# Kernel optimization log

Hardware: AMD Instinct MI355X
Metric: run time of the kernel (lower is better)

Reference implementation:

```python
import jax, jax.numpy as jnp
import numpy as np

INF = 1e38  # matches torch source constant


def setup_inputs() -> dict:
    key = jax.random.key(0)
    k1, k2, k3 = jax.random.split(key, 3)
    B, N, D = 16, 2048, 512
    query = jax.random.normal(k1, (B, N, D), dtype=jnp.float32)
    # nn.Linear(dims, dims, bias=False): weight [out, in] = [D, D]
    W_in = jax.random.normal(k2, (D, D), dtype=jnp.float32) * (1.0 / np.sqrt(D))
    # nn.Linear(2*dims, dims, bias=False): weight [D, 2D]
    W_out = jax.random.normal(k3, (D, 2 * D), dtype=jnp.float32) * (1.0 / np.sqrt(2 * D))
    return {"query": query, "W_in": W_in, "W_out": W_out}


def reference(query, W_in, W_out):
    B, N, D = query.shape
    # linear_in: y = x @ W^T
    q = jnp.einsum("bnd,ed->bne", query, W_in)  # [B, N, D]
    # full QK^T scores
    scores = jnp.einsum("bnd,bmd->bnm", q, q)  # [B, N, N]
    # torch: scores[:, triu_mask] = -INF  -> mask upper triangle INCLUDING diagonal
    mask = jnp.triu(jnp.ones((N, N), dtype=bool))
    scores = jnp.where(mask, -INF, scores)
    weights = jax.nn.softmax(scores, axis=-1)
    # row 0 is all -INF -> softmax gives uniform; torch zeroes it explicitly
    weights = weights.at[:, 0, :].set(0.0)
    mix = jnp.einsum("bnm,bmd->bnd", weights, q)  # [B, N, D]
    combined = jnp.concatenate([mix, q], axis=-1)  # [B, N, 2D]
    # linear_out (no activation since activation=None)
    output = jnp.einsum("bnc,dc->bnd", combined, W_out)  # [B, N, D]
    return output
```

## Files before the change

kernel.cpp:

```cpp
#include <hip/hip_runtime.h>

typedef _Float16 f16;
typedef _Float16 half8 __attribute__((ext_vector_type(8)));
typedef _Float16 half4 __attribute__((ext_vector_type(4)));
typedef float floatx4 __attribute__((ext_vector_type(4)));

#define MFMA16(a, b, c) __builtin_amdgcn_mfma_f32_16x16x32_f16(a, b, c, 0, 0, 0)

#define PHASE_WAIT_8()  do { asm volatile("s_waitcnt vmcnt(8)" ::: "memory"); \
    __builtin_amdgcn_sched_barrier(0); __builtin_amdgcn_s_barrier(); } while (0)
#define PHASE_WAIT_0()  do { asm volatile("s_waitcnt vmcnt(0)" ::: "memory"); \
    __builtin_amdgcn_sched_barrier(0); __builtin_amdgcn_s_barrier(); } while (0)

__device__ __forceinline__ void gload16(const void* g, void* l) {
    __builtin_amdgcn_global_load_lds((const __attribute__((address_space(1))) void*)g,
                                     (__attribute__((address_space(3))) void*)l, 16, 0, 0);
}

__global__ __launch_bounds__(256) void k_cvt(const float* __restrict__ query,
                                             const float* __restrict__ Wi,
                                             const float* __restrict__ Wo,
                                             f16* __restrict__ q16,
                                             f16* __restrict__ W16)
{
    int i = blockIdx.x * 256 + threadIdx.x;
    const float4* src;
    f16* dst;
    if (i < 4194304) { src = (const float4*)query + i; dst = q16 + (size_t)i * 4; }
    else if (i < 4259840) { int j = i - 4194304; src = (const float4*)Wi + j; dst = W16 + (size_t)j * 4; }
    else { int j = i - 4259840; src = (const float4*)Wo + j; dst = W16 + 262144 + (size_t)j * 4; }
    float4 v = *src;
    half4 h = {(f16)v.x, (f16)v.y, (f16)v.z, (f16)v.w};
    *reinterpret_cast<half4*>(dst) = h;
}

__global__ __launch_bounds__(256) void k_qin(const f16* __restrict__ q16,
                                             const f16* __restrict__ W16,
                                             f16* __restrict__ comb,
                                             f16* __restrict__ qT)
{
    __shared__ char sm[65536];
    const int tid = threadIdx.x, lane = tid & 63, w = tid >> 6;
    const int l15 = lane & 15, quad = lane >> 4;
    const int id = blockIdx.x, xcd = id & 7, u = id >> 3;
    const int mbase = (xcd * 32 + (u >> 2)) * 128;
    const int nbase = (u & 3) * 128;
    const int wm = (w & 1) * 64, wn = (w >> 1) * 64;
    const int ia = wm >> 4, jb = wn >> 4;

    floatx4 acc[4][4];
#pragma unroll
    for (int i = 0; i < 4; ++i)
#pragma unroll
        for (int j = 0; j < 4; ++j) acc[i][j] = (floatx4)0.f;

    auto STAGE = [&](int k0, int bsel) {
        f16* At = (f16*)(sm + bsel * 32768);
        f16* Bt = At + 8192;
#pragma unroll
        for (int jr = 0; jr < 4; ++jr) {
            int bi = jr * 4 + w, i2 = bi >> 1, s = bi & 1;
            gload16(q16 + (size_t)(mbase + i2 * 16 + l15) * 512 + k0 + s * 32 + quad * 8, At + bi * 512);
            gload16(W16 + (size_t)(nbase + i2 * 16 + l15) * 512 + k0 + s * 32 + quad * 8, Bt + bi * 512);
        }
    };

    STAGE(0, 0);
    STAGE(64, 1);
    for (int it = 0; it < 8; ++it) {
        const int cur = it & 1;
        if (it < 7) PHASE_WAIT_8(); else PHASE_WAIT_0();
        f16* At = (f16*)(sm + cur * 32768);
        f16* Bt = At + 8192;
#pragma unroll
        for (int s = 0; s < 2; ++s) {
            half8 a[4], bf[4];
#pragma unroll
            for (int i = 0; i < 4; ++i)
                a[i] = *reinterpret_cast<half8*>(At + ((ia + i) * 2 + s) * 512 + lane * 8);
#pragma unroll
            for (int j = 0; j < 4; ++j)
                bf[j] = *reinterpret_cast<half8*>(Bt + ((jb + j) * 2 + s) * 512 + lane * 8);
#pragma unroll
            for (int i = 0; i < 4; ++i)
#pragma unroll
                for (int j = 0; j < 4; ++j)
                    acc[i][j] = MFMA16(a[i], bf[j], acc[i][j]);
        }
        __builtin_amdgcn_s_barrier();
        if (it + 2 < 8) STAGE((it + 2) * 64, cur);
    }
    const int bb = mbase >> 11, tb = mbase & 2047;
    f16* ct = (f16*)sm;
#pragma unroll
    for (int i = 0; i < 4; ++i)
#pragma unroll
        for (int j = 0; j < 4; ++j)
#pragma unroll
            for (int r = 0; r < 4; ++r)
                ct[(wm + i * 16 + quad * 4 + r) * 136 + wn + j * 16 + l15] = (f16)acc[i][j][r];
    __syncthreads();
#pragma unroll
    for (int it = 0; it < 8; ++it) {
        int c = it * 256 + tid, r = c >> 4, c8 = (c & 15) << 3;
        *reinterpret_cast<half8*>(comb + (size_t)(mbase + r) * 1024 + 512 + nbase + c8) =
            *reinterpret_cast<half8*>(ct + r * 136 + c8);
    }
    __syncthreads();
#pragma unroll
    for (int i = 0; i < 4; ++i)
#pragma unroll
        for (int j = 0; j < 4; ++j) {
            half4 h = {(f16)acc[i][j][0], (f16)acc[i][j][1], (f16)acc[i][j][2], (f16)acc[i][j][3]};
            *reinterpret_cast<half4*>(ct + (wn + j * 16 + l15) * 136 + wm + i * 16 + quad * 4) = h;
        }
    __syncthreads();
#pragma unroll
    for (int it = 0; it < 8; ++it) {
        int c = it * 256 + tid, dd = c >> 4, tc = (c & 15) << 3;
        *reinterpret_cast<half8*>(qT + ((size_t)bb * 512 + nbase + dd) * 2048 + tb + tc) =
            *reinterpret_cast<half8*>(ct + dd * 136 + tc);
    }
}

__global__ __launch_bounds__(256) void k_sgemmsm(const f16* __restrict__ comb,
                                                 f16* __restrict__ Pd,
                                                 float* __restrict__ Mt,
                                                 float* __restrict__ Lt)
{
    __shared__ char sm[65536];
    const int tid = threadIdx.x, lane = tid & 63, w = tid >> 6;
    const int l15 = lane & 15, quad = lane >> 4;
    const int wm = (w & 1) * 64, wn = (w >> 1) * 64;
    const int ia = wm >> 4, jb = wn >> 4;

    int bx = blockIdx.y, mt = 0;
    while ((mt + 1) * (mt + 2) / 2 <= bx) ++mt;
    const int nt = bx - mt * (mt + 1) / 2;
    const int b = blockIdx.x;
    const f16* qa = comb + ((size_t)b * 2048 + mt * 128) * 1024 + 512;
    const f16* qb = comb + ((size_t)b * 2048 + nt * 128) * 1024 + 512;

    floatx4 acc[4][4];
#pragma unroll
    for (int i = 0; i < 4; ++i)
#pragma unroll
        for (int j = 0; j < 4; ++j) acc[i][j] = (floatx4)0.f;

    auto STAGE = [&](int k0, int bsel) {
        f16* At = (f16*)(sm + bsel * 32768);
        f16* Bt = At + 8192;
#pragma unroll
        for (int jr = 0; jr < 4; ++jr) {
            int bi = jr * 4 + w, i2 = bi >> 1, s = bi & 1;
            gload16(qa + (size_t)(i2 * 16 + l15) * 1024 + k0 + s * 32 + quad * 8, At + bi * 512);
            gload16(qb + (size_t)(i2 * 16 + l15) * 1024 + k0 + s * 32 + quad * 8, Bt + bi * 512);
        }
    };

    STAGE(0, 0);
    STAGE(64, 1);
    for (int it = 0; it < 8; ++it) {
        const int cur = it & 1;
        if (it < 7) PHASE_WAIT_8(); else PHASE_WAIT_0();
        f16* At = (f16*)(sm + cur * 32768);
        f16* Bt = At + 8192;
#pragma unroll
        for (int s = 0; s < 2; ++s) {
            half8 a[4], bf[4];
#pragma unroll
            for (int i = 0; i < 4; ++i)
                a[i] = *reinterpret_cast<half8*>(At + ((ia + i) * 2 + s) * 512 + lane * 8);
#pragma unroll
            for (int j = 0; j < 4; ++j)
                bf[j] = *reinterpret_cast<half8*>(Bt + ((jb + j) * 2 + s) * 512 + lane * 8);
#pragma unroll
            for (int i = 0; i < 4; ++i)
#pragma unroll
                for (int j = 0; j < 4; ++j)
                    acc[i][j] = MFMA16(a[i], bf[j], acc[i][j]);
        }
        __builtin_amdgcn_s_barrier();
        if (it + 2 < 8) STAGE((it + 2) * 64, cur);
    }

    const bool diag = (nt == mt);
    f16* ct = (f16*)sm;
    float* redm = (float*)(sm + 40960);
    float* reds = (float*)(sm + 43008);
    const int hb = w & 1;

    float wmax[4][4];
#pragma unroll
    for (int i = 0; i < 4; ++i)
#pragma unroll
        for (int r = 0; r < 4; ++r) {
            const int rowl = wm + i * 16 + quad * 4 + r;
            float mm = -1e38f;
#pragma unroll
            for (int j = 0; j < 4; ++j) {
                float v = acc[i][j][r];
                if (diag && (wn + j * 16 + l15) >= rowl) v = -1e38f;
                mm = fmaxf(mm, v);
            }
            mm = fmaxf(mm, __shfl_xor(mm, 1));
            mm = fmaxf(mm, __shfl_xor(mm, 2));
            mm = fmaxf(mm, __shfl_xor(mm, 4));
            mm = fmaxf(mm, __shfl_xor(mm, 8));
            wmax[i][r] = mm;
        }
    if (l15 == 0)
#pragma unroll
        for (int i = 0; i < 4; ++i)
#pragma unroll
            for (int r = 0; r < 4; ++r)
                redm[w * 64 + i * 16 + quad * 4 + r] = wmax[i][r];
    __syncthreads();

#pragma unroll
    for (int i = 0; i < 4; ++i)
#pragma unroll
        for (int r = 0; r < 4; ++r) {
            const int idx = i * 16 + quad * 4 + r;
            const int rowl = wm + idx;
            const float m = fmaxf(redm[hb * 64 + idx], redm[(hb + 2) * 64 + idx]);
            float ssum = 0.f;
#pragma unroll
            for (int j = 0; j < 4; ++j) {
                const int col = wn + j * 16 + l15;
                const bool valid = !diag || (col < rowl);
                float e = valid ? __expf(acc[i][j][r] - m) : 0.f;
                ssum += e;
                ct[rowl * 136 + col] = (f16)e;
            }
            ssum += __shfl_xor(ssum, 1);
            ssum += __shfl_xor(ssum, 2);
            ssum += __shfl_xor(ssum, 4);
            ssum += __shfl_xor(ssum, 8);
            wmax[i][r] = ssum;
        }
    if (l15 == 0)
#pragma unroll
        for (int i = 0; i < 4; ++i)
#pragma unroll
            for (int r = 0; r < 4; ++r)
                reds[w * 64 + i * 16 + quad * 4 + r] = wmax[i][r];
    __syncthreads();

    if (tid < 128) {
        const int h2 = tid >> 6, i2 = tid & 63;
        const float mm = fmaxf(redm[h2 * 64 + i2], redm[(h2 + 2) * 64 + i2]);
        const float ll = reds[h2 * 64 + i2] + reds[(h2 + 2) * 64 + i2];
        const size_t o = (((size_t)b * 16 + nt) << 11) + mt * 128 + tid;
        Mt[o] = mm;
        Lt[o] = ll;
    }
    f16* Pt = Pd + ((size_t)(b * 136 + bx) << 14);
#pragma unroll
    for (int itp = 0; itp < 8; ++itp) {
        int c = itp * 256 + tid, r_ = c >> 4, c8 = (c & 15) << 3;
        *reinterpret_cast<half8*>(Pt + r_ * 128 + c8) =
            *reinterpret_cast<half8*>(ct + r_ * 136 + c8);
    }
}

__global__ __launch_bounds__(256) void k_stats(float* Mt, const float* __restrict__ Lt)
{
    const int b = blockIdx.x, row = blockIdx.y * 256 + threadIdx.x;
    const int mtr = row >> 7;
    float mv[16], lv[16];
    for (int t = 0; t <= mtr; ++t) {
        const size_t o = (((size_t)b * 16 + t) << 11) + row;
        mv[t] = Mt[o];
        lv[t] = Lt[o];
    }
    float M = -1e38f;
    for (int t = 0; t <= mtr; ++t) M = fmaxf(M, mv[t]);
    float l = 0.f;
    for (int t = 0; t <= mtr; ++t) l += lv[t] * __expf(mv[t] - M);
    const float invl = (l > 0.f) ? 1.f / l : 0.f;
    for (int t = 0; t <= mtr; ++t)
        Mt[(((size_t)b * 16 + t) << 11) + row] = __expf(mv[t] - M) * invl;
}

__global__ __launch_bounds__(256) void k_pscale(f16* __restrict__ Pd,
                                               const float* __restrict__ Ft)
{
    int bx = blockIdx.y, mt = 0;
    while ((mt + 1) * (mt + 2) / 2 <= bx) ++mt;
    const int nt = bx - mt * (mt + 1) / 2;
    const int b = blockIdx.x;
    const int tid = threadIdx.x;
    const int row = tid >> 1, c0 = (tid & 1) * 64;
    const float Fv = Ft[(((size_t)b * 16 + nt) << 11) + mt * 128 + row];
    f16* Pt = Pd + ((size_t)(b * 136 + bx) << 14) + (size_t)row * 128 + c0;
#pragma unroll
    for (int c = 0; c < 8; ++c) {
        half8 h = *reinterpret_cast<half8*>(Pt + c * 8);
#pragma unroll
        for (int e = 0; e < 8; ++e) h[e] = (f16)((float)h[e] * Fv);
        *reinterpret_cast<half8*>(Pt + c * 8) = h;
    }
}

__global__ __launch_bounds__(256) void k_pv(const f16* __restrict__ Pd,
                                            const f16* __restrict__ qT,
                                            f16* __restrict__ comb)
{
    __shared__ char sm[65536];
    const int tid = threadIdx.x, lane = tid & 63, w = tid >> 6;
    const int l15 = lane & 15, quad = lane >> 4;
    const int wm = (w & 1) * 64, wn = (w >> 1) * 64;
    const int ia = wm >> 4, jb = wn >> 4;
    const int id = blockIdx.x;
    const int p = id & 7, nb = (id >> 3) & 3, b = id >> 5;
    const f16* Pdb = Pd + ((size_t)b * 136 << 14);
    const f16* qTb = qT + ((size_t)b * 512 + nb * 128) * 2048;

    for (int t = 0; t < 2; ++t) {
        const int mt = t ? (15 - p) : p;
        const int tb0 = mt * (mt + 1) / 2;
        const int kit = (mt + 1) * 2;

        floatx4 acc[4][4];
#pragma unroll
        for (int i = 0; i < 4; ++i)
#pragma unroll
            for (int j = 0; j < 4; ++j) acc[i][j] = (floatx4)0.f;

        auto STAGE = [&](int it, int bsel) {
            f16* At = (f16*)(sm + bsel * 32768);
            f16* Bt = At + 8192;
            const int k0 = it * 64;
#pragma unroll
            for (int jr = 0; jr < 4; ++jr) {
                int bi = jr * 4 + w, i2 = bi >> 1, s = bi & 1;
                gload16(Pdb + ((size_t)(tb0 + (k0 >> 7)) << 14) + (size_t)(i2 * 16 + l15) * 128
                            + (k0 & 64) + s * 32 + quad * 8,
                        At + bi * 512);
                gload16(qTb + (size_t)(i2 * 16 + l15) * 2048 + k0 + s * 32 + quad * 8, Bt + bi * 512);
            }
        };

        STAGE(0, 0);
        STAGE(1, 1);
        for (int it = 0; it < kit; ++it) {
            const int cur = it & 1;
            if (it < kit - 1) PHASE_WAIT_8(); else PHASE_WAIT_0();
            f16* At = (f16*)(sm + cur * 32768);
            f16* Bt = At + 8192;
#pragma unroll
            for (int s = 0; s < 2; ++s) {
                half8 a[4], bf[4];
#pragma unroll
                for (int i = 0; i < 4; ++i)
                    a[i] = *reinterpret_cast<half8*>(At + ((ia + i) * 2 + s) * 512 + lane * 8);
#pragma unroll
                for (int j = 0; j < 4; ++j)
                    bf[j] = *reinterpret_cast<half8*>(Bt + ((jb + j) * 2 + s) * 512 + lane * 8);
#pragma unroll
                for (int i = 0; i < 4; ++i)
#pragma unroll
                    for (int j = 0; j < 4; ++j)
                        acc[i][j] = MFMA16(a[i], bf[j], acc[i][j]);
            }
            __builtin_amdgcn_s_barrier();
            if (it + 2 < kit) STAGE(it + 2, cur);
        }

        f16* ct = (f16*)sm;
#pragma unroll
        for (int i = 0; i < 4; ++i)
#pragma unroll
            for (int j = 0; j < 4; ++j)
#pragma unroll
                for (int r = 0; r < 4; ++r)
                    ct[(wm + i * 16 + quad * 4 + r) * 136 + wn + j * 16 + l15] = (f16)acc[i][j][r];
        __syncthreads();
#pragma unroll
        for (int it = 0; it < 8; ++it) {
            int c = it * 256 + tid, r = c >> 4, c8 = (c & 15) << 3;
            *reinterpret_cast<half8*>(comb + ((size_t)b * 2048 + mt * 128 + r) * 1024 + nb * 128 + c8) =
                *reinterpret_cast<half8*>(ct + r * 136 + c8);
        }
        __syncthreads();
    }
}

__global__ __launch_bounds__(256) void k_out(const f16* __restrict__ comb,
                                             const f16* __restrict__ Wo16,
                                             float* __restrict__ out)
{
    __shared__ char sm[65536];
    const int tid = threadIdx.x, lane = tid & 63, w = tid >> 6;
    const int l15 = lane & 15, quad = lane >> 4;
    const int id = blockIdx.x, xcd = id & 7, u = id >> 3;
    const int mbase = (xcd * 32 + (u >> 2)) * 128;
    const int nbase = (u & 3) * 128;
    const int wm = (w & 1) * 64, wn = (w >> 1) * 64;
    const int ia = wm >> 4, jb = wn >> 4;

    floatx4 acc[4][4];
#pragma unroll
    for (int i = 0; i < 4; ++i)
#pragma unroll
        for (int j = 0; j < 4; ++j) acc[i][j] = (floatx4)0.f;

    auto STAGE = [&](int k0, int bsel) {
        f16* At = (f16*)(sm + bsel * 32768);
        f16* Bt = At + 8192;
#pragma unroll
        for (int jr = 0; jr < 4; ++jr) {
            int bi = jr * 4 + w, i2 = bi >> 1, s = bi & 1;
            gload16(comb + (size_t)(mbase + i2 * 16 + l15) * 1024 + k0 + s * 32 + quad * 8,
                    At + bi * 512);
            gload16(Wo16 + (size_t)(nbase + i2 * 16 + l15) * 1024 + k0 + s * 32 + quad * 8,
                    Bt + bi * 512);
        }
    };

    STAGE(0, 0);
    STAGE(64, 1);
    for (int it = 0; it < 16; ++it) {
        const int cur = it & 1;
        if (it < 15) PHASE_WAIT_8(); else PHASE_WAIT_0();
        f16* At = (f16*)(sm + cur * 32768);
        f16* Bt = At + 8192;
#pragma unroll
        for (int s = 0; s < 2; ++s) {
            half8 a[4], bf[4];
#pragma unroll
            for (int i = 0; i < 4; ++i)
                a[i] = *reinterpret_cast<half8*>(At + ((ia + i) * 2 + s) * 512 + lane * 8);
#pragma unroll
            for (int j = 0; j < 4; ++j)
                bf[j] = *reinterpret_cast<half8*>(Bt + ((jb + j) * 2 + s) * 512 + lane * 8);
#pragma unroll
            for (int i = 0; i < 4; ++i)
#pragma unroll
                for (int j = 0; j < 4; ++j)
                    acc[i][j] = MFMA16(a[i], bf[j], acc[i][j]);
        }
        __builtin_amdgcn_s_barrier();
        if (it + 2 < 16) STAGE((it + 2) * 64, cur);
    }
    float* cf = (float*)sm;
    for (int pass = 0; pass < 2; ++pass) {
        __syncthreads();
        if ((w & 1) == pass) {
#pragma unroll
            for (int i = 0; i < 4; ++i)
#pragma unroll
                for (int j = 0; j < 4; ++j)
#pragma unroll
                    for (int r = 0; r < 4; ++r)
                        cf[(i * 16 + quad * 4 + r) * 132 + wn + j * 16 + l15] = acc[i][j][r];
        }
        __syncthreads();
#pragma unroll
        for (int it = 0; it < 8; ++it) {
            int c = it * 256 + tid, row = c >> 5, c4 = (c & 31) << 2;
            __builtin_nontemporal_store(
                *reinterpret_cast<floatx4*>(cf + row * 132 + c4),
                reinterpret_cast<floatx4*>(out + (size_t)(mbase + pass * 64 + row) * 512 + nbase + c4));
        }
    }
}

extern "C" void kernel_launch(void* const* d_in, const int* in_sizes, int n_in,
                              void* d_out, int out_size, void* d_ws, size_t ws_size,
                              hipStream_t stream)
{
    const float* query = (const float*)d_in[0];
    const float* W_in  = (const float*)d_in[1];
    const float* W_out = (const float*)d_in[2];
    float* out = (float*)d_out;

    const size_t XOFF = 102236160ull;
    f16* comb = (f16*)d_ws;
    f16* qT   = comb + (size_t)32768 * 1024;
    f16* W16  = qT + (size_t)16 * 512 * 2048;
    f16* q16  = (f16*)((char*)d_ws + XOFF);
    f16* Pd   = (f16*)((char*)d_ws + XOFF);
    float* Mt = (float*)((char*)d_ws + XOFF + 71303168ull);
    float* Lt = (float*)((char*)d_ws + XOFF + 73400320ull);

    k_cvt<<<17152, 256, 0, stream>>>(query, W_in, W_out, q16, W16);
    k_qin<<<1024, 256, 0, stream>>>(q16, W16, comb, qT);
    k_sgemmsm<<<dim3(16, 136), 256, 0, stream>>>(comb, Pd, Mt, Lt);
    k_stats<<<dim3(16, 8), 256, 0, stream>>>(Mt, Lt);
    k_pscale<<<dim3(16, 136), 256, 0, stream>>>(Pd, Mt);
    k_pv<<<512, 256, 0, stream>>>(Pd, qT, comb);
    k_out<<<1024, 256, 0, stream>>>(comb, W16 + 262144, out);
}
```

Baseline: 404.5 us.

## Use 8 waves per block with 64x32 warp tiles in GEMM kernels

Switches the four MFMA GEMM kernels from 256 to 512 threads per block, halving each wave's output tile to 64x32 and its accumulator count, and splits staging loads across eight waves so the vmcnt wait drops to 4. The softmax row reductions in the score kernel now combine four column-wave partials instead of two. The aim is more waves in flight to hide LDS and global latency, in exchange for lower per-wave MFMA reuse (more LDS reads per FLOP) and more barrier participants.

```diff
diff --git a/kernel.cpp b/kernel.cpp
--- a/kernel.cpp
+++ b/kernel.cpp
@@ -7,7 +7,7 @@
 
 #define MFMA16(a, b, c) __builtin_amdgcn_mfma_f32_16x16x32_f16(a, b, c, 0, 0, 0)
 
-#define PHASE_WAIT_8()  do { asm volatile("s_waitcnt vmcnt(8)" ::: "memory"); \
+#define PHASE_WAIT_4()  do { asm volatile("s_waitcnt vmcnt(4)" ::: "memory"); \
     __builtin_amdgcn_sched_barrier(0); __builtin_amdgcn_s_barrier(); } while (0)
 #define PHASE_WAIT_0()  do { asm volatile("s_waitcnt vmcnt(0)" ::: "memory"); \
     __builtin_amdgcn_sched_barrier(0); __builtin_amdgcn_s_barrier(); } while (0)
@@ -16,6 +16,7 @@
     __builtin_amdgcn_global_load_lds((const __attribute__((address_space(1))) void*)g,
                                      (__attribute__((address_space(3))) void*)l, 16, 0, 0);
 }
+
 
 __global__ __launch_bounds__(256) void k_cvt(const float* __restrict__ query,
                                              const float* __restrict__ Wi,
@@ -34,10 +35,10 @@
     *reinterpret_cast<half4*>(dst) = h;
 }
 
-__global__ __launch_bounds__(256) void k_qin(const f16* __restrict__ q16,
-                                             const f16* __restrict__ W16,
-                                             f16* __restrict__ comb,
-                                             f16* __restrict__ qT)
+__global__ __launch_bounds__(512, 4) void k_qin(const f16* __restrict__ q16,
+                                                const f16* __restrict__ W16,
+                                                f16* __restrict__ comb,
+                                                f16* __restrict__ qT)
 {
     __shared__ char sm[65536];
     const int tid = threadIdx.x, lane = tid & 63, w = tid >> 6;
@@ -45,21 +46,21 @@
     const int id = blockIdx.x, xcd = id & 7, u = id >> 3;
     const int mbase = (xcd * 32 + (u >> 2)) * 128;
     const int nbase = (u & 3) * 128;
-    const int wm = (w & 1) * 64, wn = (w >> 1) * 64;
-    const int ia = wm >> 4, jb = wn >> 4;
-
-    floatx4 acc[4][4];
-#pragma unroll
-    for (int i = 0; i < 4; ++i)
-#pragma unroll
-        for (int j = 0; j < 4; ++j) acc[i][j] = (floatx4)0.f;
+    const int wm = (w & 1) * 64, wn = (w >> 1) * 32;
+    const int ia = (w & 1) * 4, jb = (w >> 1) * 2;
+
+    floatx4 acc[4][2];
+#pragma unroll
+    for (int i = 0; i < 4; ++i)
+#pragma unroll
+        for (int j = 0; j < 2; ++j) acc[i][j] = (floatx4)0.f;
 
     auto STAGE = [&](int k0, int bsel) {
         f16* At = (f16*)(sm + bsel * 32768);
         f16* Bt = At + 8192;
 #pragma unroll
-        for (int jr = 0; jr < 4; ++jr) {
-            int bi = jr * 4 + w, i2 = bi >> 1, s = bi & 1;
+        for (int jr = 0; jr < 2; ++jr) {
+            int bi = jr * 8 + w, i2 = bi >> 1, s = bi & 1;
             gload16(q16 + (size_t)(mbase + i2 * 16 + l15) * 512 + k0 + s * 32 + quad * 8, At + bi * 512);
             gload16(W16 + (size_t)(nbase + i2 * 16 + l15) * 512 + k0 + s * 32 + quad * 8, Bt + bi * 512);
         }
@@ -69,22 +70,22 @@
     STAGE(64, 1);
     for (int it = 0; it < 8; ++it) {
         const int cur = it & 1;
-        if (it < 7) PHASE_WAIT_8(); else PHASE_WAIT_0();
+        if (it < 7) PHASE_WAIT_4(); else PHASE_WAIT_0();
         f16* At = (f16*)(sm + cur * 32768);
         f16* Bt = At + 8192;
 #pragma unroll
         for (int s = 0; s < 2; ++s) {
-            half8 a[4], bf[4];
+            half8 a[4], bf[2];
 #pragma unroll
             for (int i = 0; i < 4; ++i)
                 a[i] = *reinterpret_cast<half8*>(At + ((ia + i) * 2 + s) * 512 + lane * 8);
 #pragma unroll
-            for (int j = 0; j < 4; ++j)
+            for (int j = 0; j < 2; ++j)
                 bf[j] = *reinterpret_cast<half8*>(Bt + ((jb + j) * 2 + s) * 512 + lane * 8);
 #pragma unroll
             for (int i = 0; i < 4; ++i)
 #pragma unroll
-                for (int j = 0; j < 4; ++j)
+                for (int j = 0; j < 2; ++j)
                     acc[i][j] = MFMA16(a[i], bf[j], acc[i][j]);
         }
         __builtin_amdgcn_s_barrier();
@@ -95,14 +96,14 @@
 #pragma unroll
     for (int i = 0; i < 4; ++i)
 #pragma unroll
-        for (int j = 0; j < 4; ++j)
+        for (int j = 0; j < 2; ++j)
 #pragma unroll
             for (int r = 0; r < 4; ++r)
                 ct[(wm + i * 16 + quad * 4 + r) * 136 + wn + j * 16 + l15] = (f16)acc[i][j][r];
     __syncthreads();
 #pragma unroll
-    for (int it = 0; it < 8; ++it) {
-        int c = it * 256 + tid, r = c >> 4, c8 = (c & 15) << 3;
+    for (int it = 0; it < 4; ++it) {
+        int c = it * 512 + tid, r = c >> 4, c8 = (c & 15) << 3;
         *reinterpret_cast<half8*>(comb + (size_t)(mbase + r) * 1024 + 512 + nbase + c8) =
             *reinterpret_cast<half8*>(ct + r * 136 + c8);
     }
@@ -110,29 +111,29 @@
 #pragma unroll
     for (int i = 0; i < 4; ++i)
 #pragma unroll
-        for (int j = 0; j < 4; ++j) {
+        for (int j = 0; j < 2; ++j) {
             half4 h = {(f16)acc[i][j][0], (f16)acc[i][j][1], (f16)acc[i][j][2], (f16)acc[i][j][3]};
             *reinterpret_cast<half4*>(ct + (wn + j * 16 + l15) * 136 + wm + i * 16 + quad * 4) = h;
         }
     __syncthreads();
 #pragma unroll
-    for (int it = 0; it < 8; ++it) {
-        int c = it * 256 + tid, dd = c >> 4, tc = (c & 15) << 3;
+    for (int it = 0; it < 4; ++it) {
+        int c = it * 512 + tid, dd = c >> 4, tc = (c & 15) << 3;
         *reinterpret_cast<half8*>(qT + ((size_t)bb * 512 + nbase + dd) * 2048 + tb + tc) =
             *reinterpret_cast<half8*>(ct + dd * 136 + tc);
     }
 }
 
-__global__ __launch_bounds__(256) void k_sgemmsm(const f16* __restrict__ comb,
-                                                 f16* __restrict__ Pd,
-                                                 float* __restrict__ Mt,
-                                                 float* __restrict__ Lt)
+__global__ __launch_bounds__(512, 4) void k_sgemmsm(const f16* __restrict__ comb,
+                                                    f16* __restrict__ Pd,
+                                                    float* __restrict__ Mt,
+                                                    float* __restrict__ Lt)
 {
     __shared__ char sm[65536];
     const int tid = threadIdx.x, lane = tid & 63, w = tid >> 6;
     const int l15 = lane & 15, quad = lane >> 4;
-    const int wm = (w & 1) * 64, wn = (w >> 1) * 64;
-    const int ia = wm >> 4, jb = wn >> 4;
+    const int wm = (w & 1) * 64, wn = (w >> 1) * 32;
+    const int ia = (w & 1) * 4, jb = (w >> 1) * 2;
 
     int bx = blockIdx.y, mt = 0;
     while ((mt + 1) * (mt + 2) / 2 <= bx) ++mt;
@@ -141,18 +142,18 @@
     const f16* qa = comb + ((size_t)b * 2048 + mt * 128) * 1024 + 512;
     const f16* qb = comb + ((size_t)b * 2048 + nt * 128) * 1024 + 512;
 
-    floatx4 acc[4][4];
-#pragma unroll
-    for (int i = 0; i < 4; ++i)
-#pragma unroll
-        for (int j = 0; j < 4; ++j) acc[i][j] = (floatx4)0.f;
+    floatx4 acc[4][2];
+#pragma unroll
+    for (int i = 0; i < 4; ++i)
+#pragma unroll
+        for (int j = 0; j < 2; ++j) acc[i][j] = (floatx4)0.f;
 
     auto STAGE = [&](int k0, int bsel) {
         f16* At = (f16*)(sm + bsel * 32768);
         f16* Bt = At + 8192;
 #pragma unroll
-        for (int jr = 0; jr < 4; ++jr) {
-            int bi = jr * 4 + w, i2 = bi >> 1, s = bi & 1;
+        for (int jr = 0; jr < 2; ++jr) {
+            int bi = jr * 8 + w, i2 = bi >> 1, s = bi & 1;
             gload16(qa + (size_t)(i2 * 16 + l15) * 1024 + k0 + s * 32 + quad * 8, At + bi * 512);
             gload16(qb + (size_t)(i2 * 16 + l15) * 1024 + k0 + s * 32 + quad * 8, Bt + bi * 512);
         }
@@ -162,22 +163,22 @@
     STAGE(64, 1);
     for (int it = 0; it < 8; ++it) {
         const int cur = it & 1;
-        if (it < 7) PHASE_WAIT_8(); else PHASE_WAIT_0();
+        if (it < 7) PHASE_WAIT_4(); else PHASE_WAIT_0();
         f16* At = (f16*)(sm + cur * 32768);
         f16* Bt = At + 8192;
 #pragma unroll
         for (int s = 0; s < 2; ++s) {
-            half8 a[4], bf[4];
+            half8 a[4], bf[2];
 #pragma unroll
             for (int i = 0; i < 4; ++i)
                 a[i] = *reinterpret_cast<half8*>(At + ((ia + i) * 2 + s) * 512 + lane * 8);
 #pragma unroll
-            for (int j = 0; j < 4; ++j)
+            for (int j = 0; j < 2; ++j)
                 bf[j] = *reinterpret_cast<half8*>(Bt + ((jb + j) * 2 + s) * 512 + lane * 8);
 #pragma unroll
             for (int i = 0; i < 4; ++i)
 #pragma unroll
-                for (int j = 0; j < 4; ++j)
+                for (int j = 0; j < 2; ++j)
                     acc[i][j] = MFMA16(a[i], bf[j], acc[i][j]);
         }
         __builtin_amdgcn_s_barrier();
@@ -186,8 +187,8 @@
 
     const bool diag = (nt == mt);
     f16* ct = (f16*)sm;
-    float* redm = (float*)(sm + 40960);
-    float* reds = (float*)(sm + 43008);
+    float* redm = (float*)(sm + 34816);
+    float* reds = (float*)(sm + 36864);
     const int hb = w & 1;
 
     float wmax[4][4];
@@ -198,7 +199,7 @@
             const int rowl = wm + i * 16 + quad * 4 + r;
             float mm = -1e38f;
 #pragma unroll
-            for (int j = 0; j < 4; ++j) {
+            for (int j = 0; j < 2; ++j) {
                 float v = acc[i][j][r];
                 if (diag && (wn + j * 16 + l15) >= rowl) v = -1e38f;
                 mm = fmaxf(mm, v);
@@ -223,10 +224,11 @@
         for (int r = 0; r < 4; ++r) {
             const int idx = i * 16 + quad * 4 + r;
             const int rowl = wm + idx;
-            const float m = fmaxf(redm[hb * 64 + idx], redm[(hb + 2) * 64 + idx]);
+            const float m = fmaxf(fmaxf(redm[hb * 64 + idx], redm[(hb + 2) * 64 + idx]),
+                                  fmaxf(redm[(hb + 4) * 64 + idx], redm[(hb + 6) * 64 + idx]));
             float ssum = 0.f;
 #pragma unroll
-            for (int j = 0; j < 4; ++j) {
+            for (int j = 0; j < 2; ++j) {
                 const int col = wn + j * 16 + l15;
                 const bool valid = !diag || (col < rowl);
                 float e = valid ? __expf(acc[i][j][r] - m) : 0.f;
@@ -249,16 +251,18 @@
 
     if (tid < 128) {
         const int h2 = tid >> 6, i2 = tid & 63;
-        const float mm = fmaxf(redm[h2 * 64 + i2], redm[(h2 + 2) * 64 + i2]);
-        const float ll = reds[h2 * 64 + i2] + reds[(h2 + 2) * 64 + i2];
+        const float mm = fmaxf(fmaxf(redm[h2 * 64 + i2], redm[(h2 + 2) * 64 + i2]),
+                               fmaxf(redm[(h2 + 4) * 64 + i2], redm[(h2 + 6) * 64 + i2]));
+        const float ll = (reds[h2 * 64 + i2] + reds[(h2 + 2) * 64 + i2])
+                       + (reds[(h2 + 4) * 64 + i2] + reds[(h2 + 6) * 64 + i2]);
         const size_t o = (((size_t)b * 16 + nt) << 11) + mt * 128 + tid;
         Mt[o] = mm;
         Lt[o] = ll;
     }
     f16* Pt = Pd + ((size_t)(b * 136 + bx) << 14);
 #pragma unroll
-    for (int itp = 0; itp < 8; ++itp) {
-        int c = itp * 256 + tid, r_ = c >> 4, c8 = (c & 15) << 3;
+    for (int itp = 0; itp < 4; ++itp) {
+        int c = itp * 512 + tid, r_ = c >> 4, c8 = (c & 15) << 3;
         *reinterpret_cast<half8*>(Pt + r_ * 128 + c8) =
             *reinterpret_cast<half8*>(ct + r_ * 136 + c8);
     }
@@ -303,15 +307,15 @@
     }
 }
 
-__global__ __launch_bounds__(256) void k_pv(const f16* __restrict__ Pd,
-                                            const f16* __restrict__ qT,
-                                            f16* __restrict__ comb)
+__global__ __launch_bounds__(512, 4) void k_pv(const f16* __restrict__ Pd,
+                                               const f16* __restrict__ qT,
+                                               f16* __restrict__ comb)
 {
     __shared__ char sm[65536];
     const int tid = threadIdx.x, lane = tid & 63, w = tid >> 6;
     const int l15 = lane & 15, quad = lane >> 4;
-    const int wm = (w & 1) * 64, wn = (w >> 1) * 64;
-    const int ia = wm >> 4, jb = wn >> 4;
+    const int wm = (w & 1) * 64, wn = (w >> 1) * 32;
+    const int ia = (w & 1) * 4, jb = (w >> 1) * 2;
     const int id = blockIdx.x;
     const int p = id & 7, nb = (id >> 3) & 3, b = id >> 5;
     const f16* Pdb = Pd + ((size_t)b * 136 << 14);
@@ -322,19 +326,19 @@
         const int tb0 = mt * (mt + 1) / 2;
         const int kit = (mt + 1) * 2;
 
-        floatx4 acc[4][4];
+        floatx4 acc[4][2];
 #pragma unroll
         for (int i = 0; i < 4; ++i)
 #pragma unroll
-            for (int j = 0; j < 4; ++j) acc[i][j] = (floatx4)0.f;
+            for (int j = 0; j < 2; ++j) acc[i][j] = (floatx4)0.f;
 
         auto STAGE = [&](int it, int bsel) {
             f16* At = (f16*)(sm + bsel * 32768);
             f16* Bt = At + 8192;
             const int k0 = it * 64;
 #pragma unroll
-            for (int jr = 0; jr < 4; ++jr) {
-                int bi = jr * 4 + w, i2 = bi >> 1, s = bi & 1;
+            for (int jr = 0; jr < 2; ++jr) {
+                int bi = jr * 8 + w, i2 = bi >> 1, s = bi & 1;
                 gload16(Pdb + ((size_t)(tb0 + (k0 >> 7)) << 14) + (size_t)(i2 * 16 + l15) * 128
                             + (k0 & 64) + s * 32 + quad * 8,
                         At + bi * 512);
@@ -346,22 +350,22 @@
         STAGE(1, 1);
         for (int it = 0; it < kit; ++it) {
             const int cur = it & 1;
-            if (it < kit - 1) PHASE_WAIT_8(); else PHASE_WAIT_0();
+            if (it < kit - 1) PHASE_WAIT_4(); else PHASE_WAIT_0();
             f16* At = (f16*)(sm + cur * 32768);
             f16* Bt = At + 8192;
 #pragma unroll
             for (int s = 0; s < 2; ++s) {
-                half8 a[4], bf[4];
+                half8 a[4], bf[2];
 #pragma unroll
                 for (int i = 0; i < 4; ++i)
                     a[i] = *reinterpret_cast<half8*>(At + ((ia + i) * 2 + s) * 512 + lane * 8);
 #pragma unroll
-                for (int j = 0; j < 4; ++j)
+                for (int j = 0; j < 2; ++j)
                     bf[j] = *reinterpret_cast<half8*>(Bt + ((jb + j) * 2 + s) * 512 + lane * 8);
 #pragma unroll
                 for (int i = 0; i < 4; ++i)
 #pragma unroll
-                    for (int j = 0; j < 4; ++j)
+                    for (int j = 0; j < 2; ++j)
                         acc[i][j] = MFMA16(a[i], bf[j], acc[i][j]);
             }
             __builtin_amdgcn_s_barrier();
@@ -372,14 +376,14 @@
 #pragma unroll
         for (int i = 0; i < 4; ++i)
 #pragma unroll
-            for (int j = 0; j < 4; ++j)
+            for (int j = 0; j < 2; ++j)
 #pragma unroll
                 for (int r = 0; r < 4; ++r)
                     ct[(wm + i * 16 + quad * 4 + r) * 136 + wn + j * 16 + l15] = (f16)acc[i][j][r];
         __syncthreads();
 #pragma unroll
-        for (int it = 0; it < 8; ++it) {
-            int c = it * 256 + tid, r = c >> 4, c8 = (c & 15) << 3;
+        for (int it = 0; it < 4; ++it) {
+            int c = it * 512 + tid, r = c >> 4, c8 = (c & 15) << 3;
             *reinterpret_cast<half8*>(comb + ((size_t)b * 2048 + mt * 128 + r) * 1024 + nb * 128 + c8) =
                 *reinterpret_cast<half8*>(ct + r * 136 + c8);
         }
@@ -387,9 +391,9 @@
     }
 }
 
-__global__ __launch_bounds__(256) void k_out(const f16* __restrict__ comb,
-                                             const f16* __restrict__ Wo16,
-                                             float* __restrict__ out)
+__global__ __launch_bounds__(512, 4) void k_out(const f16* __restrict__ comb,
+                                                const f16* __restrict__ Wo16,
+                                                float* __restrict__ out)
 {
     __shared__ char sm[65536];
     const int tid = threadIdx.x, lane = tid & 63, w = tid >> 6;
@@ -397,21 +401,21 @@
     const int id = blockIdx.x, xcd = id & 7, u = id >> 3;
     const int mbase = (xcd * 32 + (u >> 2)) * 128;
     const int nbase = (u & 3) * 128;
-    const int wm = (w & 1) * 64, wn = (w >> 1) * 64;
-    const int ia = wm >> 4, jb = wn >> 4;
-
-    floatx4 acc[4][4];
-#pragma unroll
-    for (int i = 0; i < 4; ++i)
-#pragma unroll
-        for (int j = 0; j < 4; ++j) acc[i][j] = (floatx4)0.f;
+    const int wn = (w >> 1) * 32;
+    const int ia = (w & 1) * 4, jb = (w >> 1) * 2;
+
+    floatx4 acc[4][2];
+#pragma unroll
+    for (int i = 0; i < 4; ++i)
+#pragma unroll
+        for (int j = 0; j < 2; ++j) acc[i][j] = (floatx4)0.f;
 
     auto STAGE = [&](int k0, int bsel) {
         f16* At = (f16*)(sm + bsel * 32768);
         f16* Bt = At + 8192;
 #pragma unroll
-        for (int jr = 0; jr < 4; ++jr) {
-            int bi = jr * 4 + w, i2 = bi >> 1, s = bi & 1;
+        for (int jr = 0; jr < 2; ++jr) {
+            int bi = jr * 8 + w, i2 = bi >> 1, s = bi & 1;
             gload16(comb + (size_t)(mbase + i2 * 16 + l15) * 1024 + k0 + s * 32 + quad * 8,
                     At + bi * 512);
             gload16(Wo16 + (size_t)(nbase + i2 * 16 + l15) * 1024 + k0 + s * 32 + quad * 8,
@@ -423,22 +427,22 @@
     STAGE(64, 1);
     for (int it = 0; it < 16; ++it) {
         const int cur = it & 1;
-        if (it < 15) PHASE_WAIT_8(); else PHASE_WAIT_0();
+        if (it < 15) PHASE_WAIT_4(); else PHASE_WAIT_0();
         f16* At = (f16*)(sm + cur * 32768);
         f16* Bt = At + 8192;
 #pragma unroll
         for (int s = 0; s < 2; ++s) {
-            half8 a[4], bf[4];
+            half8 a[4], bf[2];
 #pragma unroll
             for (int i = 0; i < 4; ++i)
                 a[i] = *reinterpret_cast<half8*>(At + ((ia + i) * 2 + s) * 512 + lane * 8);
 #pragma unroll
-            for (int j = 0; j < 4; ++j)
+            for (int j = 0; j < 2; ++j)
                 bf[j] = *reinterpret_cast<half8*>(Bt + ((jb + j) * 2 + s) * 512 + lane * 8);
 #pragma unroll
             for (int i = 0; i < 4; ++i)
 #pragma unroll
-                for (int j = 0; j < 4; ++j)
+                for (int j = 0; j < 2; ++j)
                     acc[i][j] = MFMA16(a[i], bf[j], acc[i][j]);
         }
         __builtin_amdgcn_s_barrier();
@@ -451,15 +455,15 @@
 #pragma unroll
             for (int i = 0; i < 4; ++i)
 #pragma unroll
-                for (int j = 0; j < 4; ++j)
+                for (int j = 0; j < 2; ++j)
 #pragma unroll
                     for (int r = 0; r < 4; ++r)
                         cf[(i * 16 + quad * 4 + r) * 132 + wn + j * 16 + l15] = acc[i][j][r];
         }
         __syncthreads();
 #pragma unroll
-        for (int it = 0; it < 8; ++it) {
-            int c = it * 256 + tid, row = c >> 5, c4 = (c & 31) << 2;
+        for (int it = 0; it < 4; ++it) {
+            int c = it * 512 + tid, row = c >> 5, c4 = (c & 31) << 2;
             __builtin_nontemporal_store(
                 *reinterpret_cast<floatx4*>(cf + row * 132 + c4),
                 reinterpret_cast<floatx4*>(out + (size_t)(mbase + pass * 64 + row) * 512 + nbase + c4));
@@ -486,10 +490,10 @@
     float* Lt = (float*)((char*)d_ws + XOFF + 73400320ull);
 
     k_cvt<<<17152, 256, 0, stream>>>(query, W_in, W_out, q16, W16);
-    k_qin<<<1024, 256, 0, stream>>>(q16, W16, comb, qT);
-    k_sgemmsm<<<dim3(16, 136), 256, 0, stream>>>(comb, Pd, Mt, Lt);
+    k_qin<<<1024, 512, 0, stream>>>(q16, W16, comb, qT);
+    k_sgemmsm<<<dim3(16, 136), 512, 0, stream>>>(comb, Pd, Mt, Lt);
     k_stats<<<dim3(16, 8), 256, 0, stream>>>(Mt, Lt);
     k_pscale<<<dim3(16, 136), 256, 0, stream>>>(Pd, Mt);
-    k_pv<<<512, 256, 0, stream>>>(Pd, qT, comb);
-    k_out<<<1024, 256, 0, stream>>>(comb, W16 + 262144, out);
-}
+    k_pv<<<512, 512, 0, stream>>>(Pd, qT, comb);
+    k_out<<<1024, 512, 0, stream>>>(comb, W16 + 262144, out);
+}
```

After: 408.4 us. About the same (+1.0%).
